# Kernel optimization log

Measured on AMD Instinct MI355X. Metric: run time of the kernel, lower is better.

Reference implementation:

```python
import jax, jax.numpy as jnp
import numpy as np

B, N, D = 8, 1024, 1024
H, DQK, DV = 8, 128, 128
L, TB = 2, 128
LN_EPS = 1e-6
LOG2 = 0.69314718056


def _layer_norm(x, g, b):
    mu = jnp.mean(x, axis=-1, keepdims=True)
    var = jnp.mean(jnp.square(x - mu), axis=-1, keepdims=True)
    return (x - mu) * jax.lax.rsqrt(var + LN_EPS) * g + b


def setup_inputs() -> dict:
    key = jax.random.key(0)
    ks = jax.random.split(key, 8)
    x = 0.02 * jax.random.normal(ks[0], (B, N, D), dtype=jnp.float32)
    timestamps = jnp.sort(jax.random.randint(ks[1], (B, N), 0, 10_000_000), axis=1).astype(jnp.int64)
    lengths = jax.random.randint(ks[2], (B,), N // 4, N + 1)
    mask = (jnp.arange(N)[None, :] < lengths[:, None]).astype(jnp.float32)  # ragged prefix mask
    return {
        "x": x,
        "timestamps": timestamps,
        "mask": mask,
        "ln1_g": jnp.ones((L, D), jnp.float32),
        "ln1_b": jnp.zeros((L, D), jnp.float32),
        "w_uvqk": 0.02 * jax.random.normal(ks[3], (L, D, 2 * H * DV + 2 * H * DQK), jnp.float32),
        "b_uvqk": jnp.zeros((L, 2 * H * DV + 2 * H * DQK), jnp.float32),
        "ln2_g": jnp.ones((L, H * DV), jnp.float32),
        "ln2_b": jnp.zeros((L, H * DV), jnp.float32),
        "w_o": 0.02 * jax.random.normal(ks[4], (L, H * DV, D), jnp.float32),
        "b_o": jnp.zeros((L, D), jnp.float32),
        "pos_w": 0.02 * jax.random.normal(ks[5], (2 * N - 1,), jnp.float32),
        "ts_w": 0.02 * jax.random.normal(ks[6], (TB + 1,), jnp.float32),
    }


def _forward(x, timestamps, mask, ln1_g, ln1_b, w_uvqk, b_uvqk, ln2_g, ln2_b, w_o, b_o, pos_w, ts_w):
    # relative position bias: pos_w[(n - m) + N - 1]
    i = jnp.arange(N)
    rel_pos = pos_w[jnp.clip(i[:, None] - i[None, :] + N - 1, 0, 2 * N - 2)]  # [N, N]
    # bucketized relative time bias (log2 bucketization, detached indices)
    ext = jnp.concatenate([timestamps, timestamps[:, -1:]], axis=1)  # [B, N+1]
    delta = ext[:, 1:, None] - ext[:, None, :-1]  # [B, N, N]
    bucket = jnp.clip(
        (jnp.log(jnp.clip(jnp.abs(delta).astype(jnp.float32), 1.0, None)) / LOG2).astype(jnp.int32),
        0, TB)
    rab = rel_pos[None, :, :] + ts_w[bucket]  # [B, N, N]
    # causal * key-validity mask (invalid_attn_mask = 1 - triu; jagged padding is zero)
    amask = jnp.tril(jnp.ones((N, N), x.dtype))[None] * mask[:, None, :]  # [B, N, N]
    x = x * mask[..., None]
    for l in range(L):
        h = _layer_norm(x, ln1_g[l], ln1_b[l])
        uvqk = jax.nn.silu(h @ w_uvqk[l] + b_uvqk[l])  # [B, N, 4096]
        u = uvqk[..., : H * DV]
        v = uvqk[..., H * DV: 2 * H * DV].reshape(B, N, H, DV)
        q = uvqk[..., 2 * H * DV: 2 * H * DV + H * DQK].reshape(B, N, H, DQK)
        k = uvqk[..., 2 * H * DV + H * DQK:].reshape(B, N, H, DQK)
        attn = jax.nn.silu(jnp.einsum('bnhd,bmhd->bhnm', q, k) + rab[:, None]) / N
        attn = attn * amask[:, None]
        o = jnp.einsum('bhnm,bmhd->bnhd', attn, v).reshape(B, N, H * DV)
        x = x + (_layer_norm(o, ln2_g[l], ln2_b[l]) * u) @ w_o[l] + b_o[l]
    # F.normalize(p=2)
    ue = x / jnp.clip(jnp.linalg.norm(x, axis=-1, keepdims=True), 1e-12)
    lengths = mask.sum(axis=1).astype(jnp.int32)  # [B]
    last = ue[jnp.arange(B), lengths - 1]  # gather last valid token, [B, D]
    avg = (ue * mask[..., None]).sum(axis=1) / lengths[:, None].astype(ue.dtype)
    pooled = 0.5 * (last + avg)
    pooled = pooled / jnp.clip(jnp.linalg.norm(pooled, axis=-1, keepdims=True), 1e-12)
    return pooled


def reference(x, timestamps, mask, ln1_g, ln1_b, w_uvqk, b_uvqk, ln2_g, ln2_b, w_o, b_o, pos_w, ts_w):
    return _forward(x, timestamps, mask, ln1_g, ln1_b, w_uvqk, b_uvqk, ln2_g, ln2_b, w_o, b_o, pos_w, ts_w)
```

## Files before the change

kernel.cpp:

```cpp
#include <hip/hip_runtime.h>
#include <hip/hip_bf16.h>
#include <cstdint>
#include <cstddef>


#define BB   8
#define NNN  1024
#define DDD  1024
#define HHH  8
#define DVV  128
#define CCC  4096
#define TBK  128

typedef __bf16 bf8_t  __attribute__((ext_vector_type(8)));
typedef float  f4_t   __attribute__((ext_vector_type(4)));

__device__ __forceinline__ float bf2f(ushort u) {
  union { uint i; float f; } v; v.i = ((uint)u) << 16; return v.f;
}
__device__ __forceinline__ ushort f2bf(float f) {
  __hip_bfloat16 h = __float2bfloat16(f);
  return *(ushort*)&h;
}

__device__ __forceinline__ float block_reduce_sum(float v, float* sm) {
#pragma unroll
  for (int o = 32; o > 0; o >>= 1) v += __shfl_down(v, o, 64);
  int lane = threadIdx.x & 63;
  int wid  = threadIdx.x >> 6;
  __syncthreads();
  if (lane == 0) sm[wid] = v;
  __syncthreads();
  int nw = blockDim.x >> 6;
  float r = (threadIdx.x < nw) ? sm[threadIdx.x] : 0.f;
#pragma unroll
  for (int o = 8; o > 0; o >>= 1) r += __shfl_down(r, o, 64);
  if (threadIdx.x == 0) sm[0] = r;
  __syncthreads();
  return sm[0];
}

__global__ __launch_bounds__(1024) void len_k(const float* __restrict__ mask,
                                              int* __restrict__ lenp) {
  __shared__ float sm[16];
  int b = blockIdx.x;
  float m = mask[(size_t)b * NNN + threadIdx.x];
  float s = block_reduce_sum(m, sm);
  if (threadIdx.x == 0) lenp[b] = (int)(s + 0.5f);
}

__global__ __launch_bounds__(256) void mask_x_k(const float* __restrict__ x,
                                                const float* __restrict__ mask,
                                                float* __restrict__ xb) {
  size_t i4 = (size_t)blockIdx.x * 256 + threadIdx.x;
  size_t row = i4 >> 8;
  float m = mask[row];
  float4 v = ((const float4*)x)[i4];
  v.x *= m; v.y *= m; v.z *= m; v.w *= m;
  ((float4*)xb)[i4] = v;
}

__global__ __launch_bounds__(256) void wconv_k(const float* __restrict__ W,
                                               ushort* __restrict__ Wt,
                                               int K, int Nn) {
  __shared__ float t[32][33];
  int k0 = blockIdx.x * 32, n0 = blockIdx.y * 32;
  int tx = threadIdx.x & 31, ty = threadIdx.x >> 5;
  for (int r = ty; r < 32; r += 8)
    t[r][tx] = W[(size_t)(k0 + r) * Nn + n0 + tx];
  __syncthreads();
  for (int r = ty; r < 32; r += 8)
    Wt[(size_t)(n0 + r) * K + k0 + tx] = f2bf(t[tx][r]);
}

__global__ __launch_bounds__(256) void rab_k(const int* __restrict__ ts,
                                             const float* __restrict__ pos_w,
                                             const float* __restrict__ ts_w,
                                             const int* __restrict__ lenp,
                                             ushort* __restrict__ rabb) {
  int jt = blockIdx.x, it = blockIdx.y, b = blockIdx.z;
  if (jt > it) return;
  int len = lenp[b];
  if (it * 128 >= len || jt * 128 >= len) return;
  int j = jt * 128 + (threadIdx.x & 127);
  int half = threadIdx.x >> 7;
  int tsj = ts[(size_t)b * NNN + j];
  for (int rr = 0; rr < 64; ++rr) {
    int i = it * 128 + rr * 2 + half;
    int ii = i + 1; if (ii > NNN - 1) ii = NNN - 1;
    int tsi = ts[(size_t)b * NNN + ii];
    float af = fabsf((float)(tsi - tsj));
    af = fmaxf(af, 1.f);
    int bkt = (int)__log2f(af);
    bkt = min(max(bkt, 0), TBK);
    float rab = pos_w[i - j + NNN - 1] + ts_w[bkt];
    rabb[((size_t)b * NNN + i) * NNN + j] = f2bf(rab);
  }
}

__global__ __launch_bounds__(256) void ln_k(const float* __restrict__ X,
                                            const float* __restrict__ g,
                                            const float* __restrict__ bsh,
                                            const float* __restrict__ umat,
                                            int ustride,
                                            const int* __restrict__ lenp,
                                            ushort* __restrict__ Y) {
  __shared__ float sm[16];
  size_t row = blockIdx.x;
  if (((int)row & 1023) >= lenp[row >> 10]) return;
  const float* xr = X + row * DDD;
  int d = threadIdx.x * 4;
  float4 xv = *(const float4*)(xr + d);
  float s = xv.x + xv.y + xv.z + xv.w;
  s = block_reduce_sum(s, sm);
  float mu = s * (1.f / 1024.f);
  float d0 = xv.x - mu, d1 = xv.y - mu, d2 = xv.z - mu, d3 = xv.w - mu;
  float ss = d0 * d0 + d1 * d1 + d2 * d2 + d3 * d3;
  ss = block_reduce_sum(ss, sm);
  float rs = rsqrtf(ss * (1.f / 1024.f) + 1e-6f);
  float y0 = d0 * rs * g[d + 0] + bsh[d + 0];
  float y1 = d1 * rs * g[d + 1] + bsh[d + 1];
  float y2 = d2 * rs * g[d + 2] + bsh[d + 2];
  float y3 = d3 * rs * g[d + 3] + bsh[d + 3];
  if (umat != nullptr) {
    const float* ur = umat + row * (size_t)ustride + d;
    y0 *= ur[0]; y1 *= ur[1]; y2 *= ur[2]; y3 *= ur[3];
  }
  ushort tmp[4] = { f2bf(y0), f2bf(y1), f2bf(y2), f2bf(y3) };
  *(uint2*)(Y + row * DDD + d) = *(uint2*)tmp;
}

template <int MODE>
__global__ __launch_bounds__(256) void gemm_bf_k(const ushort* __restrict__ A,
                                                 const ushort* __restrict__ Bt,
                                                 const float* __restrict__ bias,
                                                 float* __restrict__ C,
                                                 ushort* __restrict__ Cb,
                                                 const int* __restrict__ lenp,
                                                 int K, int Nn) {
  __shared__ alignas(16) ushort As[128 * 32];
  __shared__ alignas(16) ushort Bs[128 * 32];
  int m0 = blockIdx.y * 128, n0 = blockIdx.x * 128;
  if ((m0 & 1023) >= lenp[m0 >> 10]) return;
  int tid = threadIdx.x;
  int wave = tid >> 6, lane = tid & 63;
  int quad = lane >> 4, l16 = lane & 15;
  int wm = wave >> 1, wn = wave & 1;

  f4_t acc[4][4] = {};

  int r_l = tid >> 2;
  int p   = tid & 3;

  for (int k0 = 0; k0 < K; k0 += 32) {
    __syncthreads();
#pragma unroll
    for (int g = 0; g < 2; ++g) {
      int row = g * 64 + r_l;
      int q = (p - (row >> 1)) & 3;
      __builtin_amdgcn_global_load_lds(
          (const __attribute__((address_space(1))) void*)(A + (size_t)(m0 + row) * K + k0 + q * 8),
          (__attribute__((address_space(3))) void*)(As + (g * 64 + wave * 16) * 32),
          16, 0, 0);
      __builtin_amdgcn_global_load_lds(
          (const __attribute__((address_space(1))) void*)(Bt + (size_t)(n0 + row) * K + k0 + q * 8),
          (__attribute__((address_space(3))) void*)(Bs + (g * 64 + wave * 16) * 32),
          16, 0, 0);
    }
    __syncthreads();

    bf8_t af[4], bfr[4];
#pragma unroll
    for (int t = 0; t < 4; ++t) {
      int row = wm * 64 + t * 16 + l16;
      af[t] = *(const bf8_t*)&As[row * 32 + ((quad + (row >> 1)) & 3) * 8];
      int col = wn * 64 + t * 16 + l16;
      bfr[t] = *(const bf8_t*)&Bs[col * 32 + ((quad + (col >> 1)) & 3) * 8];
    }
#pragma unroll
    for (int i = 0; i < 4; ++i)
#pragma unroll
      for (int j = 0; j < 4; ++j)
        acc[i][j] = __builtin_amdgcn_mfma_f32_16x16x32_bf16(af[i], bfr[j],
                                                            acc[i][j], 0, 0, 0);
  }

#pragma unroll
  for (int j = 0; j < 4; ++j) {
    int col = n0 + wn * 64 + j * 16 + l16;
    float bz = bias[col];
#pragma unroll
    for (int i = 0; i < 4; ++i) {
      int rbase = m0 + wm * 64 + i * 16 + quad * 4;
#pragma unroll
      for (int r = 0; r < 4; ++r) {
        float z = acc[i][j][r] + bz;
        int row = rbase + r;
        if (MODE == 1) {
          C[(size_t)row * Nn + col] += z;
        } else {
          float s = z / (1.f + __expf(-z));
          if (col < 1024) C[(size_t)row * 1024 + col] = s;
          else Cb[(size_t)row * 3072 + (col - 1024)] = f2bf(s);
        }
      }
    }
  }
}

__global__ __launch_bounds__(256) void vt_k(const ushort* __restrict__ qkv,
                                            const int* __restrict__ lenp,
                                            ushort* __restrict__ vt) {
  __shared__ ushort t[32][33];
  int bh = blockIdx.z; int b = bh >> 3, h = bh & 7;
  int nt = blockIdx.x * 32, dt = blockIdx.y * 32;
  if (nt >= lenp[b]) return;
  int tx = threadIdx.x & 31, ty = threadIdx.x >> 5;
  for (int rr = ty; rr < 32; rr += 8)
    t[rr][tx] = qkv[(size_t)(b * NNN + nt + rr) * 3072 + h * 128 + dt + tx];
  __syncthreads();
  for (int rr = ty; rr < 32; rr += 8)
    vt[((size_t)bh * 128 + dt + rr) * NNN + nt + tx] = t[tx][rr];
}

__global__ __launch_bounds__(256, 4) void attn_mfma_k(
    const ushort* __restrict__ qkv, const ushort* __restrict__ vt,
    const ushort* __restrict__ rabb, const float* __restrict__ mask,
    const int* __restrict__ lenp, float* __restrict__ o) {
  __shared__ alignas(16) ushort Ks[64 * 128];
  __shared__ alignas(16) ushort Vs[128 * 64];
  __shared__ alignas(16) ushort Ps[64 * 64];
  int h = blockIdx.y, b = blockIdx.z;
  int qt = ((int)blockIdx.x + (int)blockIdx.y + 2 * (int)blockIdx.z) & 15;
  int n0 = qt * 64;
  if (n0 >= lenp[b]) return;
  int tid = threadIdx.x, w = tid >> 6, lane = tid & 63;
  int quad = lane >> 4, l16 = lane & 15;

  const ushort* qg0 = qkv + ((size_t)(b * NNN + n0)) * 3072 + 1024 + h * 128;
#pragma unroll
  for (int t = 0; t < 4; ++t) {
    int lrow = w * 16 + t * 4 + (lane >> 4);
    int q = ((lane & 15) - lrow) & 15;
    __builtin_amdgcn_global_load_lds(
        (const __attribute__((address_space(1))) void*)(qg0 + (size_t)lrow * 3072 + q * 8),
        (__attribute__((address_space(3))) void*)(Ks + (w * 16 + t * 4) * 128),
        16, 0, 0);
  }
  __syncthreads();
  bf8_t qf[4];
  {
    int lr = w * 16 + l16;
#pragma unroll
    for (int kk = 0; kk < 4; ++kk)
      qf[kk] = *(const bf8_t*)&Ks[lr * 128 + (((kk * 4 + quad) + lr) & 15) * 8];
  }

  f4_t oacc[8] = {};
  const ushort* kg0 = qkv + (size_t)b * NNN * 3072 + 2048 + h * 128;
  const ushort* vg0 = vt + (size_t)(b * 8 + h) * 128 * NNN;
  const ushort* rb0 = rabb + ((size_t)(b * NNN + n0 + w * 16 + quad * 4)) * NNN;
  const float* mk0 = mask + (size_t)b * NNN;
  int mtmax = qt + 1;

  for (int mt = 0; mt < mtmax; ++mt) {
    int m0 = mt * 64;
    __syncthreads();
#pragma unroll
    for (int t = 0; t < 4; ++t) {
      int lrow = w * 16 + t * 4 + (lane >> 4);
      int q = ((lane & 15) - lrow) & 15;
      __builtin_amdgcn_global_load_lds(
          (const __attribute__((address_space(1))) void*)(kg0 + (size_t)(m0 + lrow) * 3072 + q * 8),
          (__attribute__((address_space(3))) void*)(Ks + (w * 16 + t * 4) * 128),
          16, 0, 0);
    }
#pragma unroll
    for (int t = 0; t < 4; ++t) {
      int dv = w * 32 + t * 8 + (lane >> 3);
      int q = ((lane & 7) - dv) & 7;
      __builtin_amdgcn_global_load_lds(
          (const __attribute__((address_space(1))) void*)(vg0 + (size_t)dv * NNN + m0 + q * 8),
          (__attribute__((address_space(3))) void*)(Vs + (w * 32 + t * 8) * 64),
          16, 0, 0);
    }
    ushort rv[4][4];
#pragma unroll
    for (int tj = 0; tj < 4; ++tj)
#pragma unroll
      for (int r = 0; r < 4; ++r)
        rv[tj][r] = rb0[(size_t)r * NNN + m0 + tj * 16 + l16];
    __syncthreads();

    f4_t sacc[4] = {};
#pragma unroll
    for (int kk = 0; kk < 4; ++kk) {
      bf8_t kf[4];
#pragma unroll
      for (int tj = 0; tj < 4; ++tj) {
        int lr = tj * 16 + l16;
        kf[tj] = *(const bf8_t*)&Ks[lr * 128 + (((kk * 4 + quad) + lr) & 15) * 8];
      }
#pragma unroll
      for (int tj = 0; tj < 4; ++tj)
        sacc[tj] = __builtin_amdgcn_mfma_f32_16x16x32_bf16(qf[kk], kf[tj],
                                                           sacc[tj], 0, 0, 0);
    }

#pragma unroll
    for (int tj = 0; tj < 4; ++tj) {
      int m = tj * 16 + l16;
      int gj = m0 + m;
      float msc = mk0[gj] * (1.f / 1024.f);
#pragma unroll
      for (int r = 0; r < 4; ++r) {
        int q = w * 16 + quad * 4 + r;
        int gi = n0 + q;
        float z = sacc[tj][r] + bf2f(rv[tj][r]);
        float pp = z / (1.f + __expf(-z)) * msc;
        if (gj > gi) pp = 0.f;
        Ps[q * 64 + (((m >> 3) + q) & 7) * 8 + (m & 7)] = f2bf(pp);
      }
    }

#pragma unroll
    for (int kk = 0; kk < 2; ++kk) {
      bf8_t pf, vf[8];
      {
        int q = w * 16 + l16;
        pf = *(const bf8_t*)&Ps[q * 64 + (((kk * 4 + quad) + q) & 7) * 8];
      }
#pragma unroll
      for (int tj = 0; tj < 8; ++tj) {
        int dv = tj * 16 + l16;
        vf[tj] = *(const bf8_t*)&Vs[dv * 64 + (((kk * 4 + quad) + dv) & 7) * 8];
      }
#pragma unroll
      for (int tj = 0; tj < 8; ++tj)
        oacc[tj] = __builtin_amdgcn_mfma_f32_16x16x32_bf16(pf, vf[tj],
                                                           oacc[tj], 0, 0, 0);
    }
  }

#pragma unroll
  for (int tj = 0; tj < 8; ++tj) {
    int col = h * 128 + tj * 16 + l16;
#pragma unroll
    for (int r = 0; r < 4; ++r) {
      int gi = n0 + w * 16 + quad * 4 + r;
      o[((size_t)(b * NNN + gi)) * DDD + col] = oacc[tj][r];
    }
  }
}

__global__ __launch_bounds__(256) void row_stats_k(const float* __restrict__ xb,
                                                   const int* __restrict__ lenp,
                                                   float* __restrict__ invn) {
  __shared__ float sm[16];
  size_t row = blockIdx.x;
  if (((int)row & 1023) >= lenp[row >> 10]) return;
  int d = threadIdx.x * 4;
  float4 xv = *(const float4*)(xb + row * DDD + d);
  float ss = xv.x * xv.x + xv.y * xv.y + xv.z * xv.z + xv.w * xv.w;
  ss = block_reduce_sum(ss, sm);
  if (threadIdx.x == 0) invn[row] = 1.f / fmaxf(sqrtf(ss), 1e-12f);
}

__global__ __launch_bounds__(1024) void pool_partial_k(const float* __restrict__ xb,
                                                       const float* __restrict__ mask,
                                                       const float* __restrict__ invn,
                                                       const int* __restrict__ lenp,
                                                       float* __restrict__ partial) {
  int b = blockIdx.x, c = blockIdx.y, d = threadIdx.x;
  int len = lenp[b];
  float s = 0.f;
  int nbeg = c * 64;
  int nend = min(nbeg + 64, len);
  for (int n = nbeg; n < nend; ++n) {
    size_t r = (size_t)b * NNN + n;
    s += xb[r * DDD + d] * invn[r];
  }
  partial[((size_t)b * 16 + c) * DDD + d] = s;
}

__global__ __launch_bounds__(1024) void pool_final_k(const float* __restrict__ xb,
                                                     const float* __restrict__ invn,
                                                     const float* __restrict__ partial,
                                                     const int* __restrict__ lenp,
                                                     float* __restrict__ out) {
  __shared__ float sm[16];
  int b = blockIdx.x, d = threadIdx.x;
  int len = lenp[b];
  float s = 0.f;
#pragma unroll
  for (int c = 0; c < 16; ++c) s += partial[((size_t)b * 16 + c) * DDD + d];
  float avg = s / (float)len;
  size_t lr = (size_t)b * NNN + (len - 1);
  float last = xb[lr * DDD + d] * invn[lr];
  float pooled = 0.5f * (last + avg);
  float ssq = block_reduce_sum(pooled * pooled, sm);
  out[(size_t)b * DDD + d] = pooled / fmaxf(sqrtf(ssq), 1e-12f);
}

extern "C" void kernel_launch(void* const* d_in, const int* in_sizes, int n_in,
                              void* d_out, int out_size, void* d_ws, size_t ws_size,
                              hipStream_t stream) {
  const float* x      = (const float*)d_in[0];
  const int*   ts     = (const int*)d_in[1];
  const float* mask   = (const float*)d_in[2];
  const float* ln1_g  = (const float*)d_in[3];
  const float* ln1_b  = (const float*)d_in[4];
  const float* w_uvqk = (const float*)d_in[5];
  const float* b_uvqk = (const float*)d_in[6];
  const float* ln2_g  = (const float*)d_in[7];
  const float* ln2_b  = (const float*)d_in[8];
  const float* w_o    = (const float*)d_in[9];
  const float* b_o    = (const float*)d_in[10];
  const float* pos_w  = (const float*)d_in[11];
  const float* ts_w   = (const float*)d_in[12];
  float* out = (float*)d_out;

  float* ws = (float*)d_ws;
  const size_t SZ = (size_t)BB * NNN * DDD;
  float* xb   = ws;
  float* buf1 = ws + SZ;
  float* ubuf = ws + 2 * SZ;
  ushort* hbf = (ushort*)(ws + 3 * SZ);
  ushort* wuT = hbf + SZ;
  ushort* woT = wuT + 2 * (size_t)DDD * CCC;
  ushort* qkvb = woT + 2 * (size_t)DDD * DDD;
  ushort* vtb  = qkvb + (size_t)BB * NNN * 3072;
  ushort* rabb = vtb + (size_t)BB * HHH * DVV * NNN;
  float* invn = (float*)(rabb + (size_t)BB * NNN * NNN);
  float* partial = invn + (size_t)BB * NNN;
  int* lenp = (int*)(partial + (size_t)BB * 16 * DDD);

  mask_x_k<<<(BB * NNN * DDD / 4) / 256, 256, 0, stream>>>(x, mask, xb);
  len_k<<<BB, 1024, 0, stream>>>(mask, lenp);

  for (int l = 0; l < 2; ++l) {
    wconv_k<<<dim3(DDD / 32, CCC / 32), 256, 0, stream>>>(
        w_uvqk + (size_t)l * DDD * CCC, wuT + (size_t)l * CCC * DDD, DDD, CCC);
    wconv_k<<<dim3(DDD / 32, DDD / 32), 256, 0, stream>>>(
        w_o + (size_t)l * DDD * DDD, woT + (size_t)l * DDD * DDD, DDD, DDD);
  }

  rab_k<<<dim3(8, 8, BB), 256, 0, stream>>>(ts, pos_w, ts_w, lenp, rabb);

  for (int l = 0; l < 2; ++l) {
    ln_k<<<BB * NNN, 256, 0, stream>>>(xb, ln1_g + l * DDD, ln1_b + l * DDD,
                                       nullptr, 0, lenp, hbf);
    gemm_bf_k<2><<<dim3(CCC / 128, BB * NNN / 128), 256, 0, stream>>>(
        hbf, wuT + (size_t)l * CCC * DDD, b_uvqk + (size_t)l * CCC,
        ubuf, qkvb, lenp, DDD, CCC);
    vt_k<<<dim3(NNN / 32, DVV / 32, BB * HHH), 256, 0, stream>>>(qkvb, lenp, vtb);
    attn_mfma_k<<<dim3(NNN / 64, HHH, BB), 256, 0, stream>>>(
        qkvb, vtb, rabb, mask, lenp, buf1);
    ln_k<<<BB * NNN, 256, 0, stream>>>(buf1, ln2_g + l * DDD, ln2_b + l * DDD,
                                       ubuf, DDD, lenp, hbf);
    gemm_bf_k<1><<<dim3(DDD / 128, BB * NNN / 128), 256, 0, stream>>>(
        hbf, woT + (size_t)l * DDD * DDD, b_o + (size_t)l * DDD,
        xb, nullptr, lenp, DDD, DDD);
  }

  row_stats_k<<<BB * NNN, 256, 0, stream>>>(xb, lenp, invn);
  pool_partial_k<<<dim3(BB, 16), 1024, 0, stream>>>(xb, mask, invn, lenp, partial);
  pool_final_k<<<BB, 1024, 0, stream>>>(xb, invn, partial, lenp, out);
}
```

Measured before the change: 704.0 us.

## Fuse V transpose into QKV GEMM epilogue, drop mask pass, deepen K step

The QKV GEMM epilogue now writes V directly in transposed layout and Q/K into a compact 2048-wide buffer, removing the separate vt_k transpose kernel. The initial mask-multiply kernel is dropped; the first layer norm copies x into the residual buffer instead. The GEMM loads two 32-wide K slices per barrier pair, halving synchronisation count at the cost of doubled LDS usage. The transposed V stores are 4-element scattered writes, which may be less coalesced.

Result: faster. 670.0 us (-4.8%).

```diff
diff --git a/kernel.cpp b/kernel.cpp
--- a/kernel.cpp
+++ b/kernel.cpp
@@ -47,17 +47,6 @@
   float m = mask[(size_t)b * NNN + threadIdx.x];
   float s = block_reduce_sum(m, sm);
   if (threadIdx.x == 0) lenp[b] = (int)(s + 0.5f);
-}
-
-__global__ __launch_bounds__(256) void mask_x_k(const float* __restrict__ x,
-                                                const float* __restrict__ mask,
-                                                float* __restrict__ xb) {
-  size_t i4 = (size_t)blockIdx.x * 256 + threadIdx.x;
-  size_t row = i4 >> 8;
-  float m = mask[row];
-  float4 v = ((const float4*)x)[i4];
-  v.x *= m; v.y *= m; v.z *= m; v.w *= m;
-  ((float4*)xb)[i4] = v;
 }
 
 __global__ __launch_bounds__(256) void wconv_k(const float* __restrict__ W,
@@ -98,12 +87,14 @@
   }
 }
 
+template <int FIRST>
 __global__ __launch_bounds__(256) void ln_k(const float* __restrict__ X,
                                             const float* __restrict__ g,
                                             const float* __restrict__ bsh,
                                             const float* __restrict__ umat,
                                             int ustride,
                                             const int* __restrict__ lenp,
+                                            float* __restrict__ xb,
                                             ushort* __restrict__ Y) {
   __shared__ float sm[16];
   size_t row = blockIdx.x;
@@ -111,6 +102,7 @@
   const float* xr = X + row * DDD;
   int d = threadIdx.x * 4;
   float4 xv = *(const float4*)(xr + d);
+  if (FIRST) *(float4*)(xb + row * DDD + d) = xv;
   float s = xv.x + xv.y + xv.z + xv.w;
   s = block_reduce_sum(s, sm);
   float mu = s * (1.f / 1024.f);
@@ -135,11 +127,12 @@
                                                  const ushort* __restrict__ Bt,
                                                  const float* __restrict__ bias,
                                                  float* __restrict__ C,
-                                                 ushort* __restrict__ Cb,
+                                                 ushort* __restrict__ Qk,
+                                                 ushort* __restrict__ Vt,
                                                  const int* __restrict__ lenp,
                                                  int K, int Nn) {
-  __shared__ alignas(16) ushort As[128 * 32];
-  __shared__ alignas(16) ushort Bs[128 * 32];
+  __shared__ alignas(16) ushort As[2 * 128 * 32];
+  __shared__ alignas(16) ushort Bs[2 * 128 * 32];
   int m0 = blockIdx.y * 128, n0 = blockIdx.x * 128;
   if ((m0 & 1023) >= lenp[m0 >> 10]) return;
   int tid = threadIdx.x;
@@ -152,39 +145,46 @@
   int r_l = tid >> 2;
   int p   = tid & 3;
 
-  for (int k0 = 0; k0 < K; k0 += 32) {
+  for (int k0 = 0; k0 < K; k0 += 64) {
     __syncthreads();
 #pragma unroll
-    for (int g = 0; g < 2; ++g) {
-      int row = g * 64 + r_l;
-      int q = (p - (row >> 1)) & 3;
-      __builtin_amdgcn_global_load_lds(
-          (const __attribute__((address_space(1))) void*)(A + (size_t)(m0 + row) * K + k0 + q * 8),
-          (__attribute__((address_space(3))) void*)(As + (g * 64 + wave * 16) * 32),
-          16, 0, 0);
-      __builtin_amdgcn_global_load_lds(
-          (const __attribute__((address_space(1))) void*)(Bt + (size_t)(n0 + row) * K + k0 + q * 8),
-          (__attribute__((address_space(3))) void*)(Bs + (g * 64 + wave * 16) * 32),
-          16, 0, 0);
+    for (int s = 0; s < 2; ++s) {
+#pragma unroll
+      for (int g = 0; g < 2; ++g) {
+        int row = g * 64 + r_l;
+        int q = (p - (row >> 1)) & 3;
+        __builtin_amdgcn_global_load_lds(
+            (const __attribute__((address_space(1))) void*)(A + (size_t)(m0 + row) * K + k0 + s * 32 + q * 8),
+            (__attribute__((address_space(3))) void*)(As + s * 4096 + (g * 64 + wave * 16) * 32),
+            16, 0, 0);
+        __builtin_amdgcn_global_load_lds(
+            (const __attribute__((address_space(1))) void*)(Bt + (size_t)(n0 + row) * K + k0 + s * 32 + q * 8),
+            (__attribute__((address_space(3))) void*)(Bs + s * 4096 + (g * 64 + wave * 16) * 32),
+            16, 0, 0);
+      }
     }
     __syncthreads();
 
-    bf8_t af[4], bfr[4];
-#pragma unroll
-    for (int t = 0; t < 4; ++t) {
-      int row = wm * 64 + t * 16 + l16;
-      af[t] = *(const bf8_t*)&As[row * 32 + ((quad + (row >> 1)) & 3) * 8];
-      int col = wn * 64 + t * 16 + l16;
-      bfr[t] = *(const bf8_t*)&Bs[col * 32 + ((quad + (col >> 1)) & 3) * 8];
-    }
-#pragma unroll
-    for (int i = 0; i < 4; ++i)
-#pragma unroll
-      for (int j = 0; j < 4; ++j)
-        acc[i][j] = __builtin_amdgcn_mfma_f32_16x16x32_bf16(af[i], bfr[j],
-                                                            acc[i][j], 0, 0, 0);
-  }
-
+#pragma unroll
+    for (int s = 0; s < 2; ++s) {
+      bf8_t af[4], bfr[4];
+#pragma unroll
+      for (int t = 0; t < 4; ++t) {
+        int row = wm * 64 + t * 16 + l16;
+        af[t] = *(const bf8_t*)&As[s * 4096 + row * 32 + ((quad + (row >> 1)) & 3) * 8];
+        int col = wn * 64 + t * 16 + l16;
+        bfr[t] = *(const bf8_t*)&Bs[s * 4096 + col * 32 + ((quad + (col >> 1)) & 3) * 8];
+      }
+#pragma unroll
+      for (int i = 0; i < 4; ++i)
+#pragma unroll
+        for (int j = 0; j < 4; ++j)
+          acc[i][j] = __builtin_amdgcn_mfma_f32_16x16x32_bf16(af[i], bfr[j],
+                                                              acc[i][j], 0, 0, 0);
+    }
+  }
+
+  int region = n0 >> 10;
 #pragma unroll
   for (int j = 0; j < 4; ++j) {
     int col = n0 + wn * 64 + j * 16 + l16;
@@ -192,39 +192,39 @@
 #pragma unroll
     for (int i = 0; i < 4; ++i) {
       int rbase = m0 + wm * 64 + i * 16 + quad * 4;
-#pragma unroll
-      for (int r = 0; r < 4; ++r) {
-        float z = acc[i][j][r] + bz;
-        int row = rbase + r;
-        if (MODE == 1) {
-          C[(size_t)row * Nn + col] += z;
-        } else {
-          float s = z / (1.f + __expf(-z));
-          if (col < 1024) C[(size_t)row * 1024 + col] = s;
-          else Cb[(size_t)row * 3072 + (col - 1024)] = f2bf(s);
+      if (MODE == 1) {
+#pragma unroll
+        for (int r = 0; r < 4; ++r)
+          C[(size_t)(rbase + r) * Nn + col] += acc[i][j][r] + bz;
+      } else if (region == 0) {
+#pragma unroll
+        for (int r = 0; r < 4; ++r) {
+          float z = acc[i][j][r] + bz;
+          C[(size_t)(rbase + r) * 1024 + col] = z / (1.f + __expf(-z));
         }
-      }
-    }
-  }
-}
-
-__global__ __launch_bounds__(256) void vt_k(const ushort* __restrict__ qkv,
-                                            const int* __restrict__ lenp,
-                                            ushort* __restrict__ vt) {
-  __shared__ ushort t[32][33];
-  int bh = blockIdx.z; int b = bh >> 3, h = bh & 7;
-  int nt = blockIdx.x * 32, dt = blockIdx.y * 32;
-  if (nt >= lenp[b]) return;
-  int tx = threadIdx.x & 31, ty = threadIdx.x >> 5;
-  for (int rr = ty; rr < 32; rr += 8)
-    t[rr][tx] = qkv[(size_t)(b * NNN + nt + rr) * 3072 + h * 128 + dt + tx];
-  __syncthreads();
-  for (int rr = ty; rr < 32; rr += 8)
-    vt[((size_t)bh * 128 + dt + rr) * NNN + nt + tx] = t[tx][rr];
+      } else if (region == 1) {
+        int hd = col - 1024;
+        int b = m0 >> 10, nl = rbase & 1023;
+        ushort4 pk;
+        float z;
+        z = acc[i][j][0] + bz; pk.x = f2bf(z / (1.f + __expf(-z)));
+        z = acc[i][j][1] + bz; pk.y = f2bf(z / (1.f + __expf(-z)));
+        z = acc[i][j][2] + bz; pk.z = f2bf(z / (1.f + __expf(-z)));
+        z = acc[i][j][3] + bz; pk.w = f2bf(z / (1.f + __expf(-z)));
+        *(ushort4*)&Vt[((size_t)(b * 8 + (hd >> 7)) * 128 + (hd & 127)) * NNN + nl] = pk;
+      } else {
+#pragma unroll
+        for (int r = 0; r < 4; ++r) {
+          float z = acc[i][j][r] + bz;
+          Qk[(size_t)(rbase + r) * 2048 + (col - 2048)] = f2bf(z / (1.f + __expf(-z)));
+        }
+      }
+    }
+  }
 }
 
 __global__ __launch_bounds__(256, 4) void attn_mfma_k(
-    const ushort* __restrict__ qkv, const ushort* __restrict__ vt,
+    const ushort* __restrict__ qk, const ushort* __restrict__ vt,
     const ushort* __restrict__ rabb, const float* __restrict__ mask,
     const int* __restrict__ lenp, float* __restrict__ o) {
   __shared__ alignas(16) ushort Ks[64 * 128];
@@ -237,13 +237,13 @@
   int tid = threadIdx.x, w = tid >> 6, lane = tid & 63;
   int quad = lane >> 4, l16 = lane & 15;
 
-  const ushort* qg0 = qkv + ((size_t)(b * NNN + n0)) * 3072 + 1024 + h * 128;
+  const ushort* qg0 = qk + ((size_t)(b * NNN + n0)) * 2048 + h * 128;
 #pragma unroll
   for (int t = 0; t < 4; ++t) {
     int lrow = w * 16 + t * 4 + (lane >> 4);
     int q = ((lane & 15) - lrow) & 15;
     __builtin_amdgcn_global_load_lds(
-        (const __attribute__((address_space(1))) void*)(qg0 + (size_t)lrow * 3072 + q * 8),
+        (const __attribute__((address_space(1))) void*)(qg0 + (size_t)lrow * 2048 + q * 8),
         (__attribute__((address_space(3))) void*)(Ks + (w * 16 + t * 4) * 128),
         16, 0, 0);
   }
@@ -257,7 +257,7 @@
   }
 
   f4_t oacc[8] = {};
-  const ushort* kg0 = qkv + (size_t)b * NNN * 3072 + 2048 + h * 128;
+  const ushort* kg0 = qk + (size_t)b * NNN * 2048 + 1024 + h * 128;
   const ushort* vg0 = vt + (size_t)(b * 8 + h) * 128 * NNN;
   const ushort* rb0 = rabb + ((size_t)(b * NNN + n0 + w * 16 + quad * 4)) * NNN;
   const float* mk0 = mask + (size_t)b * NNN;
@@ -271,7 +271,7 @@
       int lrow = w * 16 + t * 4 + (lane >> 4);
       int q = ((lane & 15) - lrow) & 15;
       __builtin_amdgcn_global_load_lds(
-          (const __attribute__((address_space(1))) void*)(kg0 + (size_t)(m0 + lrow) * 3072 + q * 8),
+          (const __attribute__((address_space(1))) void*)(kg0 + (size_t)(m0 + lrow) * 2048 + q * 8),
           (__attribute__((address_space(3))) void*)(Ks + (w * 16 + t * 4) * 128),
           16, 0, 0);
     }
@@ -367,7 +367,6 @@
 }
 
 __global__ __launch_bounds__(1024) void pool_partial_k(const float* __restrict__ xb,
-                                                       const float* __restrict__ mask,
                                                        const float* __restrict__ invn,
                                                        const int* __restrict__ lenp,
                                                        float* __restrict__ partial) {
@@ -428,14 +427,13 @@
   ushort* hbf = (ushort*)(ws + 3 * SZ);
   ushort* wuT = hbf + SZ;
   ushort* woT = wuT + 2 * (size_t)DDD * CCC;
-  ushort* qkvb = woT + 2 * (size_t)DDD * DDD;
-  ushort* vtb  = qkvb + (size_t)BB * NNN * 3072;
+  ushort* qkb = woT + 2 * (size_t)DDD * DDD;
+  ushort* vtb = qkb + (size_t)BB * NNN * 2048;
   ushort* rabb = vtb + (size_t)BB * HHH * DVV * NNN;
   float* invn = (float*)(rabb + (size_t)BB * NNN * NNN);
   float* partial = invn + (size_t)BB * NNN;
   int* lenp = (int*)(partial + (size_t)BB * 16 * DDD);
 
-  mask_x_k<<<(BB * NNN * DDD / 4) / 256, 256, 0, stream>>>(x, mask, xb);
   len_k<<<BB, 1024, 0, stream>>>(mask, lenp);
 
   for (int l = 0; l < 2; ++l) {
@@ -448,22 +446,27 @@
   rab_k<<<dim3(8, 8, BB), 256, 0, stream>>>(ts, pos_w, ts_w, lenp, rabb);
 
   for (int l = 0; l < 2; ++l) {
-    ln_k<<<BB * NNN, 256, 0, stream>>>(xb, ln1_g + l * DDD, ln1_b + l * DDD,
-                                       nullptr, 0, lenp, hbf);
+    if (l == 0)
+      ln_k<1><<<BB * NNN, 256, 0, stream>>>(x, ln1_g, ln1_b, nullptr, 0,
+                                            lenp, xb, hbf);
+    else
+      ln_k<0><<<BB * NNN, 256, 0, stream>>>(xb, ln1_g + l * DDD,
+                                            ln1_b + l * DDD, nullptr, 0,
+                                            lenp, nullptr, hbf);
     gemm_bf_k<2><<<dim3(CCC / 128, BB * NNN / 128), 256, 0, stream>>>(
         hbf, wuT + (size_t)l * CCC * DDD, b_uvqk + (size_t)l * CCC,
-        ubuf, qkvb, lenp, DDD, CCC);
-    vt_k<<<dim3(NNN / 32, DVV / 32, BB * HHH), 256, 0, stream>>>(qkvb, lenp, vtb);
+        ubuf, qkb, vtb, lenp, DDD, CCC);
     attn_mfma_k<<<dim3(NNN / 64, HHH, BB), 256, 0, stream>>>(
-        qkvb, vtb, rabb, mask, lenp, buf1);
-    ln_k<<<BB * NNN, 256, 0, stream>>>(buf1, ln2_g + l * DDD, ln2_b + l * DDD,
-                                       ubuf, DDD, lenp, hbf);
+        qkb, vtb, rabb, mask, lenp, buf1);
+    ln_k<0><<<BB * NNN, 256, 0, stream>>>(buf1, ln2_g + l * DDD,
+                                          ln2_b + l * DDD, ubuf, DDD,
+                                          lenp, nullptr, hbf);
     gemm_bf_k<1><<<dim3(DDD / 128, BB * NNN / 128), 256, 0, stream>>>(
         hbf, woT + (size_t)l * DDD * DDD, b_o + (size_t)l * DDD,
-        xb, nullptr, lenp, DDD, DDD);
+        xb, nullptr, nullptr, lenp, DDD, DDD);
   }
 
   row_stats_k<<<BB * NNN, 256, 0, stream>>>(xb, lenp, invn);
-  pool_partial_k<<<dim3(BB, 16), 1024, 0, stream>>>(xb, mask, invn, lenp, partial);
+  pool_partial_k<<<dim3(BB, 16), 1024, 0, stream>>>(xb, invn, lenp, partial);
   pool_final_k<<<BB, 1024, 0, stream>>>(xb, invn, partial, lenp, out);
 }
```
